# Optimization experiments

Measured on AMD Instinct MI355X. Metric: run time of the kernel, lower is better.

## Reference

```python
import jax, jax.numpy as jnp
import numpy as np

NH, NL, NPNT = 8, 4, 4          # heads, levels, points
NQ, BS, NK, D, DFFN = 100, 8, 18, 256, 1024
SPATIAL = np.array([[92, 92], [46, 46], [23, 23], [12, 12]], np.int32)
LEN_MEM = int((SPATIAL[:, 0] * SPATIAL[:, 1]).sum())  # 11253


def _layernorm(x, g, b):
    m = x.mean(-1, keepdims=True)
    v = ((x - m) ** 2).mean(-1, keepdims=True)
    return (x - m) / jnp.sqrt(v + 1e-5) * g + b


def _mha(xq, xk, xv, in_w, in_b, out_w, out_b):
    # torch nn.MultiheadAttention semantics, inputs (S, B, D)
    S, B, d = xq.shape
    dh = d // NH
    wq, wk, wv = jnp.split(in_w, 3, axis=0)
    bq, bk, bv = jnp.split(in_b, 3, axis=0)
    def proj(x, w, b):
        return (x @ w.T + b).reshape(x.shape[0], B, NH, dh).transpose(1, 2, 0, 3)
    q = proj(xq, wq, bq) * (1.0 / np.sqrt(dh))
    k = proj(xk, wk, bk)
    v = proj(xv, wv, bv)
    att = jax.nn.softmax(jnp.einsum('bhqd,bhkd->bhqk', q, k), axis=-1)
    o = jnp.einsum('bhqk,bhkd->bhqd', att, v).transpose(2, 0, 1, 3).reshape(S, B, d)
    return o @ out_w.T + out_b


def _bilinear(v_l, loc):
    # v_l: (bs,H,W,NH,dh); loc: (bs,Lq,NH,P,2) normalized [0,1]
    # matches F.grid_sample(align_corners=False, padding_mode='zeros')
    bs, H, W, nh, dh = v_l.shape
    x = loc[..., 0] * W - 0.5
    y = loc[..., 1] * H - 0.5
    x0 = jnp.floor(x); y0 = jnp.floor(y)
    lx = x - x0; ly = y - y0
    b_idx = jnp.arange(bs)[:, None, None, None]
    h_idx = jnp.arange(nh)[None, None, :, None]
    def corner(xa, ya, w):
        valid = (xa >= 0) & (xa < W) & (ya >= 0) & (ya < H)
        xi = jnp.clip(xa, 0, W - 1).astype(jnp.int32)
        yi = jnp.clip(ya, 0, H - 1).astype(jnp.int32)
        return v_l[b_idx, yi, xi, h_idx] * (w * valid)[..., None]
    return (corner(x0, y0, (1 - lx) * (1 - ly)) + corner(x0 + 1, y0, lx * (1 - ly))
            + corner(x0, y0 + 1, (1 - lx) * ly) + corner(x0 + 1, y0 + 1, lx * ly))


def _msda(q, rp, mem, pad_mask, ss, off_w, off_b, aw_w, aw_b, val_w, val_b, outp_w, outp_b):
    bs, Lq, d = q.shape
    dh = d // NH
    value = mem @ val_w.T + val_b
    value = jnp.where(pad_mask[..., None], 0.0, value).reshape(bs, -1, NH, dh)
    off = (q @ off_w.T + off_b).reshape(bs, Lq, NH, NL, NPNT, 2)
    aw = jax.nn.softmax((q @ aw_w.T + aw_b).reshape(bs, Lq, NH, NL * NPNT), -1)
    aw = aw.reshape(bs, Lq, NH, NL, NPNT)
    wh = jnp.asarray(ss[:, ::-1].copy(), jnp.float32)  # offset normalizer (W, H)
    loc = rp[:, :, None, :, None, :] + off / wh[None, None, None, :, None, :]
    out = jnp.zeros((bs, Lq, NH, dh), q.dtype)
    start = 0
    for l in range(NL):
        H, W = int(ss[l, 0]), int(ss[l, 1])
        v_l = value[:, start:start + H * W].reshape(bs, H, W, NH, dh)
        start += H * W
        samp = _bilinear(v_l, loc[:, :, :, l])          # (bs,Lq,NH,P,dh)
        out = out + (samp * aw[:, :, :, l, :, None]).sum(3)
    return out.reshape(bs, Lq, d) @ outp_w.T + outp_b


def _forward(tgt_pose, pos, ref_points, memory, w_in_w, w_in_b, w_out_w, w_out_b,
             a_in_w, a_in_b, a_out_w, a_out_b, off_w, off_b, aw_w, aw_b,
             val_w, val_b, outp_w, outp_b, wn_g, wn_b, an_g, an_b,
             n1_g, n1_b, n2_g, n2_b, l1_w, l1_b, l2_w, l2_b,
             spatial_shapes, level_start_index, padding_mask):
    ss = np.asarray(jax.device_get(spatial_shapes))
    nq, bs, nk, d = tgt_pose.shape
    # within-group self-attn over the nk keypoint tokens.
    # NOTE: with_pos_embed mutates tgt_pose in place in the torch code, so
    # q = k = v = tgt + pos and the residual also uses tgt + pos (faithful).
    t = tgt_pose + pos
    x = t.reshape(nq * bs, nk, d).transpose(1, 0, 2)   # (nk, nq*bs, d)
    a1 = _mha(x, x, x, w_in_w, w_in_b, w_out_w, w_out_b)
    t = _layernorm(t + a1.transpose(1, 0, 2).reshape(nq, bs, nk, d), wn_g, wn_b)
    # across-group self-attn over the nq groups
    x2 = t.reshape(nq, bs * nk, d)
    a2 = _mha(x2, x2, x2, a_in_w, a_in_b, a_out_w, a_out_b)
    t = _layernorm(t + a2.reshape(nq, bs, nk, d), an_g, an_b)
    # MSDeformAttn cross-attention (in-place pos add again, faithful)
    t = t + pos
    q = t.transpose(1, 0, 2, 3).reshape(bs, nq * nk, d)
    rp = jnp.swapaxes(ref_points, 0, 1)                # (bs, nq*nk, NL, 2)
    mem = jnp.swapaxes(memory, 0, 1)                   # (bs, LEN_MEM, d)
    c = _msda(q, rp, mem, padding_mask, ss, off_w, off_b, aw_w, aw_b,
              val_w, val_b, outp_w, outp_b)
    c = c.reshape(bs, nq, nk, d).transpose(1, 0, 2, 3)
    t = _layernorm(t + c, n1_g, n1_b)
    # FFN (dropout is identity in eval)
    h = jax.nn.relu(t @ l1_w.T + l1_b)
    return _layernorm(t + (h @ l2_w.T + l2_b), n2_g, n2_b)


def setup_inputs() -> dict:
    key = jax.random.key(0)
    ks = jax.random.split(key, 16)
    p = lambda k, shape: jax.random.normal(k, shape, jnp.float32) * 0.02
    lsi = np.concatenate([[0], np.cumsum(SPATIAL[:, 0] * SPATIAL[:, 1])[:-1]]).astype(np.int32)
    return {
        'tgt_pose': jax.random.normal(ks[0], (NQ, BS, NK, D), jnp.float32),
        'pos': jax.random.normal(ks[1], (NQ, BS, NK, D), jnp.float32),
        'ref_points': jax.random.uniform(ks[2], (NQ * NK, BS, NL, 2), jnp.float32),
        'memory': jax.random.normal(ks[3], (LEN_MEM, BS, D), jnp.float32),
        'w_in_w': p(ks[4], (3 * D, D)), 'w_in_b': jnp.zeros((3 * D,)),
        'w_out_w': p(ks[5], (D, D)), 'w_out_b': jnp.zeros((D,)),
        'a_in_w': p(ks[6], (3 * D, D)), 'a_in_b': jnp.zeros((3 * D,)),
        'a_out_w': p(ks[7], (D, D)), 'a_out_b': jnp.zeros((D,)),
        'off_w': p(ks[8], (NH * NL * NPNT * 2, D)),
        'off_b': jax.random.uniform(ks[9], (NH * NL * NPNT * 2,), jnp.float32, -2.0, 2.0),
        'aw_w': p(ks[10], (NH * NL * NPNT, D)), 'aw_b': jnp.zeros((NH * NL * NPNT,)),
        'val_w': p(ks[11], (D, D)), 'val_b': jnp.zeros((D,)),
        'outp_w': p(ks[12], (D, D)), 'outp_b': jnp.zeros((D,)),
        'wn_g': jnp.ones((D,)), 'wn_b': jnp.zeros((D,)),
        'an_g': jnp.ones((D,)), 'an_b': jnp.zeros((D,)),
        'n1_g': jnp.ones((D,)), 'n1_b': jnp.zeros((D,)),
        'n2_g': jnp.ones((D,)), 'n2_b': jnp.zeros((D,)),
        'l1_w': p(ks[13], (DFFN, D)), 'l1_b': jnp.zeros((DFFN,)),
        'l2_w': p(ks[14], (D, DFFN)), 'l2_b': jnp.zeros((D,)),
        'spatial_shapes': jnp.asarray(SPATIAL),
        'level_start_index': jnp.asarray(lsi),
        'padding_mask': jnp.zeros((BS, LEN_MEM), bool),
    }


def reference(tgt_pose, pos, ref_points, memory, w_in_w, w_in_b, w_out_w, w_out_b,
              a_in_w, a_in_b, a_out_w, a_out_b, off_w, off_b, aw_w, aw_b,
              val_w, val_b, outp_w, outp_b, wn_g, wn_b, an_g, an_b,
              n1_g, n1_b, n2_g, n2_b, l1_w, l1_b, l2_w, l2_b,
              spatial_shapes, level_start_index, padding_mask):
    return _forward(tgt_pose, pos, ref_points, memory, w_in_w, w_in_b, w_out_w, w_out_b,
                    a_in_w, a_in_b, a_out_w, a_out_b, off_w, off_b, aw_w, aw_b,
                    val_w, val_b, outp_w, outp_b, wn_g, wn_b, an_g, an_b,
                    n1_g, n1_b, n2_g, n2_b, l1_w, l1_b, l2_w, l2_b,
                    spatial_shapes, level_start_index, padding_mask)
```

## Files before the change

kernel.cpp:

```cpp
#include <hip/hip_runtime.h>
#include <math.h>

#define NH_ 8
#define D_ 256
#define NK_ 18
#define NQ_ 100
#define BS_ 8
#define LQ_ 1800
#define LEN_MEM_ 11253
#define NTOK_ 14400

typedef short bf16x8 __attribute__((ext_vector_type(8)));
typedef float f32x4 __attribute__((ext_vector_type(4)));
typedef unsigned short ushort;

__device__ inline ushort f2bf(float f) {
    unsigned int u = __builtin_bit_cast(unsigned int, f);
    unsigned int r = (u + 0x7fffu + ((u >> 16) & 1u)) >> 16;
    return (ushort)r;
}
__device__ inline float bf2f_hi(unsigned int u) {
    unsigned int i = u & 0xffff0000u;
    return __builtin_bit_cast(float, i);
}
__device__ inline float bf2f_lo(unsigned int u) {
    unsigned int i = u << 16;
    return __builtin_bit_cast(float, i);
}
__device__ inline int packbf2(float a, float b) {
    return (int)f2bf(a) | ((int)f2bf(b) << 16);
}

__global__ __launch_bounds__(256)
void wcvt_kernel(const float* s0, const float* s1, const float* s2, const float* s3,
                 const float* s4, const float* s5, const float* s6, const float* s7,
                 const float* s8, const float* s9, ushort* dst) {
    const int sizes[10] = {196608,65536,196608,65536,65536,32768,65536,65536,262144,262144};
    const int offs[10]  = {0,196608,262144,458752,524288,589824,622592,688128,753664,1015808};
    int ti = blockIdx.y;
    const float* s;
    switch (ti) {
        case 0: s = s0; break; case 1: s = s1; break; case 2: s = s2; break;
        case 3: s = s3; break; case 4: s = s4; break; case 5: s = s5; break;
        case 6: s = s6; break; case 7: s = s7; break; case 8: s = s8; break;
        default: s = s9; break;
    }
    int n = sizes[ti];
    int i = (blockIdx.x * 256 + threadIdx.x) * 8;
    if (i >= n) return;
    ushort* d = dst + offs[ti] + i;
    float4 f0 = *(const float4*)(s + i);
    float4 f1 = *(const float4*)(s + i + 4);
    int4 val;
    val.x = packbf2(f0.x, f0.y);
    val.y = packbf2(f0.z, f0.w);
    val.z = packbf2(f1.x, f1.y);
    val.w = packbf2(f1.z, f1.w);
    *(int4*)d = val;
}

__global__ __launch_bounds__(256)
void addcvt_kernel(const float* __restrict__ a, const float* __restrict__ b,
                   float* __restrict__ c, ushort* __restrict__ cbf, int n4) {
    int i = blockIdx.x * blockDim.x + threadIdx.x;
    if (i >= n4) return;
    float4 av = ((const float4*)a)[i];
    float4 bv = ((const float4*)b)[i];
    float4 cv;
    cv.x = av.x + bv.x; cv.y = av.y + bv.y; cv.z = av.z + bv.z; cv.w = av.w + bv.w;
    ((float4*)c)[i] = cv;
    uint2 p;
    p.x = (unsigned int)packbf2(cv.x, cv.y);
    p.y = (unsigned int)packbf2(cv.z, cv.w);
    *(uint2*)(cbf + (size_t)i * 4) = p;
}

template<int MODE, bool RELU, bool A_F32, bool OUT_BF16, int BN, int WAVES, int R>
__global__ __launch_bounds__(WAVES * 64)
void gemmw_kernel(const void* __restrict__ Av, const ushort* __restrict__ W,
                  const float* __restrict__ bias, void* __restrict__ Cv,
                  int M, int N, const unsigned char* __restrict__ mask) {
    constexpr int K = 256;
    constexpr int NT = BN / 16;
    __shared__ ushort Ws[32 * BN * 8];
    const int tid = threadIdx.x;
    const int m0 = blockIdx.x * (WAVES * 16 * R);
    const int n0 = blockIdx.y * BN;

    for (int c = tid; c < 32 * BN; c += WAVES * 64) {
        int kc = c & 31, n = c >> 5;
        int dst = kc * BN + (n ^ (kc & 7));
        *(int4*)(Ws + dst * 8) = *(const int4*)(W + (long)(n0 + n) * K + kc * 8);
    }
    __syncthreads();

    const int wv = tid >> 6, lane = tid & 63, fr = lane & 15, hi = lane >> 4;
    const int wm0 = m0 + wv * (16 * R);
    long arow[R];
#pragma unroll
    for (int r = 0; r < R; ++r) {
        int gr = wm0 + r * 16 + fr;
        if (gr > M - 1) gr = M - 1;
        if (MODE == 2) {
            int b = gr / LQ_; int lq = gr - b * LQ_;
            int q = lq / NK_; int kk = lq - q * NK_;
            arow[r] = (long)q * (BS_ * NK_) + b * NK_ + kk;
        } else {
            arow[r] = gr;
        }
    }

    f32x4 acc[R][NT];
#pragma unroll
    for (int r = 0; r < R; ++r)
#pragma unroll
        for (int t = 0; t < NT; ++t) acc[r][t] = f32x4{0.f, 0.f, 0.f, 0.f};

    if (A_F32) {
        const float* ap[R];
        float4 p0[R], p1[R];
#pragma unroll
        for (int r = 0; r < R; ++r) {
            ap[r] = (const float*)Av + arow[r] * (long)K + hi * 8;
            p0[r] = *(const float4*)ap[r];
            p1[r] = *(const float4*)(ap[r] + 4);
        }
#pragma unroll
        for (int ks = 0; ks < 8; ++ks) {
            bf16x8 cur[R];
#pragma unroll
            for (int r = 0; r < R; ++r) {
                int4 v;
                v.x = packbf2(p0[r].x, p0[r].y); v.y = packbf2(p0[r].z, p0[r].w);
                v.z = packbf2(p1[r].x, p1[r].y); v.w = packbf2(p1[r].z, p1[r].w);
                cur[r] = __builtin_bit_cast(bf16x8, v);
                if (ks < 7) {
                    p0[r] = *(const float4*)(ap[r] + (ks + 1) * 32);
                    p1[r] = *(const float4*)(ap[r] + (ks + 1) * 32 + 4);
                }
            }
            const int kc = ks * 4 + hi;
            const ushort* wb = Ws + ((kc * BN) + (fr ^ (kc & 7))) * 8;
#pragma unroll
            for (int t = 0; t < NT; ++t) {
                bf16x8 wf = *(const bf16x8*)(wb + t * 128);
#pragma unroll
                for (int r = 0; r < R; ++r)
                    acc[r][t] = __builtin_amdgcn_mfma_f32_16x16x32_bf16(cur[r], wf, acc[r][t], 0, 0, 0);
            }
        }
    } else {
        const ushort* ap[R];
        bf16x8 afrag[R];
#pragma unroll
        for (int r = 0; r < R; ++r) {
            ap[r] = (const ushort*)Av + arow[r] * (long)K + hi * 8;
            afrag[r] = *(const bf16x8*)ap[r];
        }
#pragma unroll
        for (int ks = 0; ks < 8; ++ks) {
            bf16x8 cur[R];
#pragma unroll
            for (int r = 0; r < R; ++r) {
                cur[r] = afrag[r];
                if (ks < 7) afrag[r] = *(const bf16x8*)(ap[r] + (ks + 1) * 32);
            }
            const int kc = ks * 4 + hi;
            const ushort* wb = Ws + ((kc * BN) + (fr ^ (kc & 7))) * 8;
#pragma unroll
            for (int t = 0; t < NT; ++t) {
                bf16x8 wf = *(const bf16x8*)(wb + t * 128);
#pragma unroll
                for (int r = 0; r < R; ++r)
                    acc[r][t] = __builtin_amdgcn_mfma_f32_16x16x32_bf16(cur[r], wf, acc[r][t], 0, 0, 0);
            }
        }
    }

#pragma unroll
    for (int r = 0; r < R; ++r) {
#pragma unroll
        for (int rr = 0; rr < 4; ++rr) {
            int gm = wm0 + r * 16 + hi * 4 + rr;
            if (gm >= M) continue;
            long orow = gm;
            bool zero = false;
            if (MODE == 1) {
                if (mask && mask[(size_t)(gm & 7) * LEN_MEM_ + (gm >> 3)]) zero = true;
            } else if (MODE == 3) {
                int b = gm / LQ_; int lq = gm - b * LQ_;
                int q = lq / NK_; int kk = lq - q * NK_;
                orow = (long)q * (BS_ * NK_) + b * NK_ + kk;
            }
#pragma unroll
            for (int t = 0; t < NT; ++t) {
                int gn = n0 + t * 16 + fr;
                float v = acc[r][t][rr] + bias[gn];
                if (RELU) v = fmaxf(v, 0.f);
                if (zero) v = 0.f;
                if (OUT_BF16) ((ushort*)Cv)[orow * (long)N + gn] = f2bf(v);
                else ((float*)Cv)[orow * (long)N + gn] = v;
            }
        }
    }
}

template<int MODE, bool RELU, bool A_F32, bool OUT_BF16>
__global__ __launch_bounds__(256)
void gemm_kernel(const void* __restrict__ Av, const ushort* __restrict__ W,
                 const float* __restrict__ bias, void* __restrict__ Cv,
                 int M, int N, int K, const unsigned char* __restrict__ mask) {
    constexpr int AST = 72;
    __shared__ ushort As[128 * AST];
    __shared__ ushort Bs[128 * AST];
    const int m0 = blockIdx.x * 128, n0 = blockIdx.y * 128;
    const int tid = threadIdx.x;
    const int w = tid >> 6, lane = tid & 63;
    const int wr = w >> 1, wc = w & 1;
    const int fr = lane & 15, hi = lane >> 4;
    f32x4 acc[4][4];
#pragma unroll
    for (int i = 0; i < 4; ++i)
#pragma unroll
        for (int j = 0; j < 4; ++j) acc[i][j] = f32x4{0.f, 0.f, 0.f, 0.f};

    const int srow = tid >> 1, shalf = tid & 1;
    long arow = 0;
    const bool avalid = (m0 + srow) < M;
    {
        int gr = m0 + srow;
        if (gr >= M) gr = M - 1;
        arow = gr;
    }

    for (int k0 = 0; k0 < K; k0 += 64) {
        ushort* ad = As + srow * AST + shalf * 32;
        if (avalid) {
            const ushort* ap = (const ushort*)Av + arow * (long)K + k0 + shalf * 32;
#pragma unroll
            for (int i = 0; i < 4; ++i) *(int4*)(ad + i * 8) = *(const int4*)(ap + i * 8);
        } else {
            int4 z = make_int4(0, 0, 0, 0);
#pragma unroll
            for (int i = 0; i < 4; ++i) *(int4*)(ad + i * 8) = z;
        }
        {
            const ushort* wp = W + (long)(n0 + srow) * K + k0 + shalf * 32;
            ushort* bd = Bs + srow * AST + shalf * 32;
#pragma unroll
            for (int i = 0; i < 4; ++i) *(int4*)(bd + i * 8) = *(const int4*)(wp + i * 8);
        }
        __syncthreads();
#pragma unroll
        for (int kb = 0; kb < 2; ++kb) {
            bf16x8 af[4], bfr[4];
#pragma unroll
            for (int i = 0; i < 4; ++i)
                af[i] = *(const bf16x8*)(As + (wr * 64 + i * 16 + fr) * AST + kb * 32 + hi * 8);
#pragma unroll
            for (int j = 0; j < 4; ++j)
                bfr[j] = *(const bf16x8*)(Bs + (wc * 64 + j * 16 + fr) * AST + kb * 32 + hi * 8);
#pragma unroll
            for (int i = 0; i < 4; ++i)
#pragma unroll
                for (int j = 0; j < 4; ++j)
                    acc[i][j] = __builtin_amdgcn_mfma_f32_16x16x32_bf16(af[i], bfr[j], acc[i][j], 0, 0, 0);
        }
        __syncthreads();
    }

#pragma unroll
    for (int i = 0; i < 4; ++i) {
#pragma unroll
        for (int r = 0; r < 4; ++r) {
            int gm = m0 + wr * 64 + i * 16 + hi * 4 + r;
            if (gm >= M) continue;
#pragma unroll
            for (int j = 0; j < 4; ++j) {
                int gn = n0 + wc * 64 + j * 16 + fr;
                float v = acc[i][j][r] + bias[gn];
                if (RELU) v = fmaxf(v, 0.f);
                if (OUT_BF16) ((ushort*)Cv)[(long)gm * N + gn] = f2bf(v);
                else ((float*)Cv)[(long)gm * N + gn] = v;
            }
        }
    }
}

template<int S, int SP, int HPB>
__global__ __launch_bounds__(256)
void mattn_kernel(const ushort* __restrict__ qkv, ushort* __restrict__ outb,
                  int rsG, int rsS) {
    constexpr int SPk = ((SP + 31) / 32) * 32;
    constexpr int KST = 40;
    constexpr int PST = SPk + 8;
    constexpr int NT = SP / 16;
    constexpr int NB = HPB * NT;
    constexpr int HB = 8 / HPB;
    __shared__ ushort KsA[HPB * SP * KST];
    __shared__ ushort VtA[HPB * 32 * PST];
    __shared__ ushort PA [HPB * SP * PST];

    const int tid = threadIdx.x;
    const int g = blockIdx.x / HB;
    const int hbase = (blockIdx.x % HB) * HPB;

    for (int idx = tid; idx < HPB * S * 4; idx += 256) {
        int hh = idx / (S * 4); int rem = idx - hh * (S * 4);
        int j = rem >> 2, q = rem & 3;
        const ushort* base = qkv + ((size_t)g * rsG + (size_t)j * rsS) * 768 + (hbase + hh) * 32 + q * 8;
        uint4 kv = *(const uint4*)(base + 256);
        ushort* kd = KsA + hh * (SP * KST) + j * KST + q * 8;
        *(uint2*)kd = make_uint2(kv.x, kv.y);
        *(uint2*)(kd + 4) = make_uint2(kv.z, kv.w);
        uint4 vv = *(const uint4*)(base + 512);
        ushort* vt = VtA + hh * (32 * PST) + j;
        unsigned int uu[4] = {vv.x, vv.y, vv.z, vv.w};
#pragma unroll
        for (int e = 0; e < 4; ++e) {
            vt[(q * 8 + e * 2    ) * PST] = (ushort)(uu[e] & 0xffff);
            vt[(q * 8 + e * 2 + 1) * PST] = (ushort)(uu[e] >> 16);
        }
    }
    for (int idx = tid; idx < HPB * 32 * (SPk - S); idx += 256) {
        int hh = idx / (32 * (SPk - S)); int rem = idx - hh * (32 * (SPk - S));
        int d = rem / (SPk - S); int c = S + rem - d * (SPk - S);
        VtA[hh * 32 * PST + d * PST + c] = 0;
    }
    if constexpr (SPk > SP) {
        constexpr int PW = SPk - SP;
        for (int idx = tid; idx < HPB * SP * PW; idx += 256) {
            int hh = idx / (SP * PW); int rem = idx - hh * (SP * PW);
            int rrow = rem / PW; int c = SP + rem - rrow * PW;
            PA[hh * SP * PST + rrow * PST + c] = 0;
        }
    }
    __syncthreads();

    const int wv = tid >> 6, lane = tid & 63, fr = lane & 15, hi = lane >> 4;
    for (int band = wv; band < NB; band += 4) {
        const int hh = band / NT, mb = band - (band / NT) * NT;
        const int h = hbase + hh;
        const ushort* Ks = KsA + hh * (SP * KST);
        const ushort* Vt = VtA + hh * (32 * PST);
        ushort* P = PA + hh * (SP * PST);

        int sq = mb * 16 + fr; if (sq > S - 1) sq = S - 1;
        bf16x8 qf = *(const bf16x8*)(qkv + ((size_t)g * rsG + (size_t)sq * rsS) * 768 + h * 32 + hi * 8);
        f32x4 sc[NT];
#pragma unroll
        for (int t = 0; t < NT; ++t) {
            bf16x8 kf = *(const bf16x8*)(Ks + (t * 16 + fr) * KST + hi * 8);
            sc[t] = __builtin_amdgcn_mfma_f32_16x16x32_bf16(qf, kf, f32x4{0.f, 0.f, 0.f, 0.f}, 0, 0, 0);
        }
#pragma unroll
        for (int t = 0; t < NT; ++t) {
            bool valid = (t * 16 + fr) < S;
#pragma unroll
            for (int r = 0; r < 4; ++r)
                sc[t][r] = valid ? sc[t][r] * 0.17677669529663687f : -1e30f;
        }
#pragma unroll
        for (int r = 0; r < 4; ++r) {
            float m = sc[0][r];
#pragma unroll
            for (int t = 1; t < NT; ++t) m = fmaxf(m, sc[t][r]);
            m = fmaxf(m, __shfl_xor(m, 1)); m = fmaxf(m, __shfl_xor(m, 2));
            m = fmaxf(m, __shfl_xor(m, 4)); m = fmaxf(m, __shfl_xor(m, 8));
            float e[NT]; float sum = 0.f;
#pragma unroll
            for (int t = 0; t < NT; ++t) { e[t] = __expf(sc[t][r] - m); sum += e[t]; }
            sum += __shfl_xor(sum, 1); sum += __shfl_xor(sum, 2);
            sum += __shfl_xor(sum, 4); sum += __shfl_xor(sum, 8);
            float inv = 1.f / sum;
            int row = mb * 16 + hi * 4 + r;
#pragma unroll
            for (int t = 0; t < NT; ++t)
                P[row * PST + t * 16 + fr] = f2bf(e[t] * inv);
        }
        f32x4 o0 = {0.f, 0.f, 0.f, 0.f}, o1 = {0.f, 0.f, 0.f, 0.f};
#pragma unroll
        for (int kb = 0; kb < SPk / 32; ++kb) {
            bf16x8 pf = *(const bf16x8*)(P + (mb * 16 + fr) * PST + kb * 32 + hi * 8);
            bf16x8 v0 = *(const bf16x8*)(Vt + fr * PST + kb * 32 + hi * 8);
            bf16x8 v1 = *(const bf16x8*)(Vt + (16 + fr) * PST + kb * 32 + hi * 8);
            o0 = __builtin_amdgcn_mfma_f32_16x16x32_bf16(pf, v0, o0, 0, 0, 0);
            o1 = __builtin_amdgcn_mfma_f32_16x16x32_bf16(pf, v1, o1, 0, 0, 0);
        }
#pragma unroll
        for (int r = 0; r < 4; ++r) {
            int s = mb * 16 + hi * 4 + r;
            if (s < S) {
                size_t ob = ((size_t)g * rsG + (size_t)s * rsS) * 256 + h * 32;
                outb[ob + fr] = f2bf(o0[r]);
                outb[ob + 16 + fr] = f2bf(o1[r]);
            }
        }
    }
}

__global__ __launch_bounds__(256)
void addln_kernel(const float* __restrict__ base, const float* __restrict__ delta,
                  const float* __restrict__ gamma, const float* __restrict__ beta,
                  const float* __restrict__ pos,
                  float* __restrict__ out, ushort* __restrict__ obf, int M) {
    int row = blockIdx.x * 4 + (threadIdx.x >> 6);
    int lane = threadIdx.x & 63;
    if (row >= M) return;
    const float* pb = base + (size_t)row * 256;
    const float* pd = delta + (size_t)row * 256;
    float v[4]; float s = 0.f;
#pragma unroll
    for (int i = 0; i < 4; ++i) { int c = lane + i * 64; v[i] = pb[c] + pd[c]; s += v[i]; }
#pragma unroll
    for (int off = 32; off; off >>= 1) s += __shfl_xor(s, off);
    float mean = s * (1.f / 256.f);
    float var = 0.f;
#pragma unroll
    for (int i = 0; i < 4; ++i) { float d = v[i] - mean; var += d * d; }
#pragma unroll
    for (int off = 32; off; off >>= 1) var += __shfl_xor(var, off);
    var *= (1.f / 256.f);
    float rstd = rsqrtf(var + 1e-5f);
#pragma unroll
    for (int i = 0; i < 4; ++i) {
        int c = lane + i * 64;
        float o = (v[i] - mean) * rstd * gamma[c] + beta[c];
        if (pos) o += pos[(size_t)row * 256 + c];
        out[(size_t)row * 256 + c] = o;
        if (obf) obf[(size_t)row * 256 + c] = f2bf(o);
    }
}

__global__ __launch_bounds__(256)
void msda_kernel(const float* __restrict__ offb, const float* __restrict__ aw,
                 const ushort* __restrict__ val, const float* __restrict__ refp,
                 const int* __restrict__ spatial, const int* __restrict__ lsi,
                 ushort* __restrict__ samp) {
    const int unit = blockIdx.x * 32 + (threadIdx.x >> 3);
    const int lane8 = threadIdx.x & 7;
    const int base8 = (threadIdx.x & 63) & 56;
    const int h = unit & 7;
    const int t = unit >> 3;
    const int lq = t % LQ_;
    const int b = t / LQ_;
    const size_t row = (size_t)b * LQ_ + lq;

    float2 lg = *(const float2*)(aw + row * 128 + h * 16 + lane8 * 2);
    float m = fmaxf(lg.x, lg.y);
    m = fmaxf(m, __shfl_xor(m, 1)); m = fmaxf(m, __shfl_xor(m, 2)); m = fmaxf(m, __shfl_xor(m, 4));
    float e0 = __expf(lg.x - m), e1 = __expf(lg.y - m);
    float s = e0 + e1;
    s += __shfl_xor(s, 1); s += __shfl_xor(s, 2); s += __shfl_xor(s, 4);
    float inv = 1.f / s;
    float w0 = e0 * inv, w1 = e1 * inv;

    float4 of = *(const float4*)(offb + row * 256 + h * 32 + lane8 * 4);

    const float* rp = refp + ((size_t)lq * BS_ + b) * 8;
    float4 rp0 = *(const float4*)rp;
    float4 rp1 = *(const float4*)(rp + 4);

    float acc[4] = {0.f, 0.f, 0.f, 0.f};

#pragma unroll 1
    for (int lvl = 0; lvl < 4; ++lvl) {
        int H = spatial[lvl * 2], W = spatial[lvl * 2 + 1];
        int st = lsi[lvl];
        float rpx = (lvl == 0) ? rp0.x : (lvl == 1) ? rp0.z : (lvl == 2) ? rp1.x : rp1.z;
        float rpy = (lvl == 0) ? rp0.y : (lvl == 1) ? rp0.w : (lvl == 2) ? rp1.y : rp1.w;
        const ushort* vb = val + ((size_t)st * 8 + b) * 256 + h * 32 + lane8 * 4;
        float fW = (float)W, fH = (float)H;
#pragma unroll
        for (int p = 0; p < 4; ++p) {
            float ox_ = (p & 1) ? of.z : of.x;
            float oy_ = (p & 1) ? of.w : of.y;
            float wp_ = (p & 1) ? w1 : w0;
            int src = base8 + lvl * 2 + (p >> 1);
            float ox  = __shfl(ox_, src);
            float oy  = __shfl(oy_, src);
            float wpt = __shfl(wp_, src);

            float x = rpx * fW + ox - 0.5f;
            float y = rpy * fH + oy - 0.5f;
            float x0f = floorf(x), y0f = floorf(y);
            float lx = x - x0f, ly = y - y0f;
            int x0 = (int)x0f, y0 = (int)y0f;
            int xc0 = min(max(x0, 0), W - 1), xc1 = min(max(x0 + 1, 0), W - 1);
            int yc0 = min(max(y0, 0), H - 1), yc1 = min(max(y0 + 1, 0), H - 1);
            float vx0 = (x0 >= 0 && x0 < W) ? 1.f : 0.f;
            float vx1 = (x0 >= -1 && x0 + 1 < W) ? 1.f : 0.f;
            float vy0 = (y0 >= 0 && y0 < H) ? 1.f : 0.f;
            float vy1 = (y0 >= -1 && y0 + 1 < H) ? 1.f : 0.f;
            float w00 = wpt * (1.f - lx) * (1.f - ly) * vx0 * vy0;
            float w10 = wpt * lx * (1.f - ly) * vx1 * vy0;
            float w01 = wpt * (1.f - lx) * ly * vx0 * vy1;
            float w11 = wpt * lx * ly * vx1 * vy1;
            uint2 u00 = *(const uint2*)(vb + (size_t)(yc0 * W + xc0) * 2048);
            uint2 u10 = *(const uint2*)(vb + (size_t)(yc0 * W + xc1) * 2048);
            uint2 u01 = *(const uint2*)(vb + (size_t)(yc1 * W + xc0) * 2048);
            uint2 u11 = *(const uint2*)(vb + (size_t)(yc1 * W + xc1) * 2048);
            acc[0] += w00 * bf2f_lo(u00.x) + w10 * bf2f_lo(u10.x)
                    + w01 * bf2f_lo(u01.x) + w11 * bf2f_lo(u11.x);
            acc[1] += w00 * bf2f_hi(u00.x) + w10 * bf2f_hi(u10.x)
                    + w01 * bf2f_hi(u01.x) + w11 * bf2f_hi(u11.x);
            acc[2] += w00 * bf2f_lo(u00.y) + w10 * bf2f_lo(u10.y)
                    + w01 * bf2f_lo(u01.y) + w11 * bf2f_lo(u11.y);
            acc[3] += w00 * bf2f_hi(u00.y) + w10 * bf2f_hi(u10.y)
                    + w01 * bf2f_hi(u01.y) + w11 * bf2f_hi(u11.y);
        }
    }
    size_t o = row * 256 + h * 32 + lane8 * 4;
    uint2 pk;
    pk.x = (unsigned int)packbf2(acc[0], acc[1]);
    pk.y = (unsigned int)packbf2(acc[2], acc[3]);
    *(uint2*)(samp + o) = pk;
}

extern "C" void kernel_launch(void* const* d_in, const int* in_sizes, int n_in,
                              void* d_out, int out_size, void* d_ws, size_t ws_size,
                              hipStream_t stream) {
    const float* tgt     = (const float*)d_in[0];
    const float* pos     = (const float*)d_in[1];
    const float* refp    = (const float*)d_in[2];
    const float* memory  = (const float*)d_in[3];
    const float* w_in_w  = (const float*)d_in[4];
    const float* w_in_b  = (const float*)d_in[5];
    const float* w_out_w = (const float*)d_in[6];
    const float* w_out_b = (const float*)d_in[7];
    const float* a_in_w  = (const float*)d_in[8];
    const float* a_in_b  = (const float*)d_in[9];
    const float* a_out_w = (const float*)d_in[10];
    const float* a_out_b = (const float*)d_in[11];
    const float* off_w   = (const float*)d_in[12];
    const float* off_b   = (const float*)d_in[13];
    const float* aw_w    = (const float*)d_in[14];
    const float* aw_b    = (const float*)d_in[15];
    const float* val_w   = (const float*)d_in[16];
    const float* val_b   = (const float*)d_in[17];
    const float* outp_w  = (const float*)d_in[18];
    const float* outp_b  = (const float*)d_in[19];
    const float* wn_g    = (const float*)d_in[20];
    const float* wn_b    = (const float*)d_in[21];
    const float* an_g    = (const float*)d_in[22];
    const float* an_b    = (const float*)d_in[23];
    const float* n1_g    = (const float*)d_in[24];
    const float* n1_b    = (const float*)d_in[25];
    const float* n2_g    = (const float*)d_in[26];
    const float* n2_b    = (const float*)d_in[27];
    const float* l1_w    = (const float*)d_in[28];
    const float* l1_b    = (const float*)d_in[29];
    const float* l2_w    = (const float*)d_in[30];
    const float* l2_b    = (const float*)d_in[31];
    const int*   spatial = (const int*)d_in[32];
    const int*   lsi     = (const int*)d_in[33];
    const unsigned char* pmask = (const unsigned char*)d_in[34];
    float* out = (float*)d_out;

    float*  T      = (float*)d_ws;
    ushort* Tbf    = (ushort*)(T + 3686400);
    ushort* B16    = Tbf + 3686400;
    ushort* CBbf   = B16 + 11059200;
    ushort* VALbf  = CBbf + 3686400;
    ushort* SAMPbf = VALbf + 23046144;
    ushort* Hbf    = SAMPbf + 3686400;
    ushort* WB     = Hbf + 14745600;
    float*  OFF    = (float*)(WB + 1277952);
    float*  AW     = OFF + 3686400;

    ushort* WB_win  = WB + 0;
    ushort* WB_wout = WB + 196608;
    ushort* WB_ain  = WB + 262144;
    ushort* WB_aout = WB + 458752;
    ushort* WB_off  = WB + 524288;
    ushort* WB_aw   = WB + 589824;
    ushort* WB_val  = WB + 622592;
    ushort* WB_outp = WB + 688128;
    ushort* WB_l1   = WB + 753664;
    ushort* WB_l2   = WB + 1015808;

    const int n4 = NTOK_ * 256 / 4;

    wcvt_kernel<<<dim3(128, 10), 256, 0, stream>>>(
        w_in_w, w_out_w, a_in_w, a_out_w, off_w, aw_w, val_w, outp_w, l1_w, l2_w, WB);
    addcvt_kernel<<<n4 / 256, 256, 0, stream>>>(tgt, pos, T, Tbf, n4);
    gemmw_kernel<0, false, false, true, 64, 4, 2><<<dim3(113, 12), 256, 0, stream>>>(
        Tbf, WB_win, w_in_b, B16, NTOK_, 768, nullptr);
    mattn_kernel<18, 32, 4><<<800 * 2, 256, 0, stream>>>(B16, CBbf, 18, 1);
    gemmw_kernel<0, false, false, false, 64, 4, 2><<<dim3(113, 4), 256, 0, stream>>>(
        CBbf, WB_wout, w_out_b, OFF, NTOK_, 256, nullptr);
    addln_kernel<<<NTOK_ / 4, 256, 0, stream>>>(T, OFF, wn_g, wn_b, nullptr, T, Tbf, NTOK_);
    gemmw_kernel<0, false, false, true, 64, 4, 2><<<dim3(113, 12), 256, 0, stream>>>(
        Tbf, WB_ain, a_in_b, B16, NTOK_, 768, nullptr);
    mattn_kernel<100, 112, 1><<<144 * 8, 256, 0, stream>>>(B16, CBbf, 1, 144);
    gemmw_kernel<0, false, false, false, 64, 4, 2><<<dim3(113, 4), 256, 0, stream>>>(
        CBbf, WB_aout, a_out_b, OFF, NTOK_, 256, nullptr);
    addln_kernel<<<NTOK_ / 4, 256, 0, stream>>>(T, OFF, an_g, an_b, pos, T, Tbf, NTOK_);
    gemmw_kernel<1, false, true, true, 128, 8, 2><<<dim3(352, 2), 512, 0, stream>>>(
        memory, WB_val, val_b, VALbf, 90024, 256, pmask);
    gemmw_kernel<2, false, false, false, 64, 4, 2><<<dim3(113, 4), 256, 0, stream>>>(
        Tbf, WB_off, off_b, OFF, NTOK_, 256, nullptr);
    gemmw_kernel<2, false, false, false, 64, 4, 2><<<dim3(113, 2), 256, 0, stream>>>(
        Tbf, WB_aw, aw_b, AW, NTOK_, 128, nullptr);
    msda_kernel<<<3600, 256, 0, stream>>>(OFF, AW, VALbf, refp, spatial, lsi, SAMPbf);
    gemmw_kernel<3, false, false, false, 64, 4, 2><<<dim3(113, 4), 256, 0, stream>>>(
        SAMPbf, WB_outp, outp_b, OFF, NTOK_, 256, nullptr);
    addln_kernel<<<NTOK_ / 4, 256, 0, stream>>>(T, OFF, n1_g, n1_b, nullptr, T, Tbf, NTOK_);
    gemmw_kernel<0, true, false, true, 64, 4, 2><<<dim3(113, 16), 256, 0, stream>>>(
        Tbf, WB_l1, l1_b, Hbf, NTOK_, 1024, nullptr);
    gemm_kernel<0, false, false, false><<<dim3(113, 2), 256, 0, stream>>>(
        Hbf, WB_l2, l2_b, OFF, NTOK_, 256, 1024, nullptr);
    addln_kernel<<<NTOK_ / 4, 256, 0, stream>>>(T, OFF, n2_g, n2_b, nullptr, out, nullptr, NTOK_);
}
```

Before: 345.9 us.

## Co-schedule value and QKV GEMMs, fuse offset/weight GEMMs, use bf16 residual deltas

Merges the large value-projection GEMM with the first self-attention in-projection GEMM into a single launch that interleaves blocks of both. Also merges the sampling-offset and attention-weight projections into one launch. The projection outputs feeding the add+LayerNorm kernels are now written in bf16, and the LayerNorm kernel is vectorised with float4 loads and stores. This cuts launch count and the traffic of the intermediate tensors, at the cost of bf16 rounding on the residual deltas and a different tile shape for the QKV GEMM.

```diff
diff --git a/kernel.cpp b/kernel.cpp
--- a/kernel.cpp
+++ b/kernel.cpp
@@ -76,16 +76,15 @@
 }
 
 template<int MODE, bool RELU, bool A_F32, bool OUT_BF16, int BN, int WAVES, int R>
-__global__ __launch_bounds__(WAVES * 64)
-void gemmw_kernel(const void* __restrict__ Av, const ushort* __restrict__ W,
-                  const float* __restrict__ bias, void* __restrict__ Cv,
-                  int M, int N, const unsigned char* __restrict__ mask) {
+__device__ __forceinline__
+void gemmw_body(int bx, int by, const void* __restrict__ Av, const ushort* __restrict__ W,
+                const float* __restrict__ bias, void* __restrict__ Cv,
+                int M, int N, const unsigned char* __restrict__ mask, ushort* Ws) {
     constexpr int K = 256;
     constexpr int NT = BN / 16;
-    __shared__ ushort Ws[32 * BN * 8];
     const int tid = threadIdx.x;
-    const int m0 = blockIdx.x * (WAVES * 16 * R);
-    const int n0 = blockIdx.y * BN;
+    const int m0 = bx * (WAVES * 16 * R);
+    const int n0 = by * BN;
 
     for (int c = tid; c < 32 * BN; c += WAVES * 64) {
         int kc = c & 31, n = c >> 5;
@@ -203,6 +202,49 @@
             }
         }
     }
+}
+
+template<int MODE, bool RELU, bool A_F32, bool OUT_BF16, int BN, int WAVES, int R>
+__global__ __launch_bounds__(WAVES * 64)
+void gemmw_kernel(const void* __restrict__ Av, const ushort* __restrict__ W,
+                  const float* __restrict__ bias, void* __restrict__ Cv,
+                  int M, int N, const unsigned char* __restrict__ mask) {
+    __shared__ ushort Ws[32 * BN * 8];
+    gemmw_body<MODE, RELU, A_F32, OUT_BF16, BN, WAVES, R>(
+        blockIdx.x, blockIdx.y, Av, W, bias, Cv, M, N, mask, Ws);
+}
+
+__global__ __launch_bounds__(512)
+void fusedqv_kernel(const float* __restrict__ memA, const ushort* __restrict__ Wv,
+                    const float* __restrict__ bv, ushort* __restrict__ Cval,
+                    const unsigned char* __restrict__ mask,
+                    const ushort* __restrict__ Aq, const ushort* __restrict__ Wq,
+                    const float* __restrict__ bq, ushort* __restrict__ Cq) {
+    __shared__ ushort Ws[32 * 128 * 8];
+    int idx = blockIdx.x;
+    int g3 = idx / 3, r3 = idx - g3 * 3;
+    if (r3 < 2) {
+        int v = g3 * 2 + r3;
+        gemmw_body<1, false, true, true, 128, 8, 2>(v >> 1, v & 1, memA, Wv, bv, Cval,
+                                                    90024, 256, mask, Ws);
+    } else {
+        int q = g3;
+        if (q < 342)
+            gemmw_body<0, false, false, true, 128, 8, 2>(q % 57, q / 57, Aq, Wq, bq, Cq,
+                                                         NTOK_, 768, nullptr, Ws);
+    }
+}
+
+__global__ __launch_bounds__(256)
+void fusedoa_kernel(const ushort* __restrict__ A,
+                    const ushort* __restrict__ Woff, const float* __restrict__ boff, float* __restrict__ Coff,
+                    const ushort* __restrict__ Waw, const float* __restrict__ baw, float* __restrict__ Caw) {
+    __shared__ ushort Ws[32 * 64 * 8];
+    int by = blockIdx.y;
+    if (by < 4)
+        gemmw_body<2, false, false, false, 64, 4, 2>(blockIdx.x, by, A, Woff, boff, Coff, NTOK_, 256, nullptr, Ws);
+    else
+        gemmw_body<2, false, false, false, 64, 4, 2>(blockIdx.x, by - 4, A, Waw, baw, Caw, NTOK_, 128, nullptr, Ws);
 }
 
 template<int MODE, bool RELU, bool A_F32, bool OUT_BF16>
@@ -400,18 +442,22 @@
 }
 
 __global__ __launch_bounds__(256)
-void addln_kernel(const float* __restrict__ base, const float* __restrict__ delta,
+void addln_kernel(const float* __restrict__ base, const ushort* __restrict__ delta,
                   const float* __restrict__ gamma, const float* __restrict__ beta,
                   const float* __restrict__ pos,
                   float* __restrict__ out, ushort* __restrict__ obf, int M) {
     int row = blockIdx.x * 4 + (threadIdx.x >> 6);
     int lane = threadIdx.x & 63;
     if (row >= M) return;
-    const float* pb = base + (size_t)row * 256;
-    const float* pd = delta + (size_t)row * 256;
-    float v[4]; float s = 0.f;
-#pragma unroll
-    for (int i = 0; i < 4; ++i) { int c = lane + i * 64; v[i] = pb[c] + pd[c]; s += v[i]; }
+    const size_t rb = (size_t)row * 256 + lane * 4;
+    float4 bv = *(const float4*)(base + rb);
+    uint2 du = *(const uint2*)(delta + rb);
+    float v[4];
+    v[0] = bv.x + bf2f_lo(du.x);
+    v[1] = bv.y + bf2f_hi(du.x);
+    v[2] = bv.z + bf2f_lo(du.y);
+    v[3] = bv.w + bf2f_hi(du.y);
+    float s = v[0] + v[1] + v[2] + v[3];
 #pragma unroll
     for (int off = 32; off; off >>= 1) s += __shfl_xor(s, off);
     float mean = s * (1.f / 256.f);
@@ -422,13 +468,24 @@
     for (int off = 32; off; off >>= 1) var += __shfl_xor(var, off);
     var *= (1.f / 256.f);
     float rstd = rsqrtf(var + 1e-5f);
-#pragma unroll
-    for (int i = 0; i < 4; ++i) {
-        int c = lane + i * 64;
-        float o = (v[i] - mean) * rstd * gamma[c] + beta[c];
-        if (pos) o += pos[(size_t)row * 256 + c];
-        out[(size_t)row * 256 + c] = o;
-        if (obf) obf[(size_t)row * 256 + c] = f2bf(o);
+    float4 gv = *(const float4*)(gamma + lane * 4);
+    float4 bev = *(const float4*)(beta + lane * 4);
+    float o[4];
+    o[0] = (v[0] - mean) * rstd * gv.x + bev.x;
+    o[1] = (v[1] - mean) * rstd * gv.y + bev.y;
+    o[2] = (v[2] - mean) * rstd * gv.z + bev.z;
+    o[3] = (v[3] - mean) * rstd * gv.w + bev.w;
+    if (pos) {
+        float4 pv = *(const float4*)(pos + rb);
+        o[0] += pv.x; o[1] += pv.y; o[2] += pv.z; o[3] += pv.w;
+    }
+    float4 ov; ov.x = o[0]; ov.y = o[1]; ov.z = o[2]; ov.w = o[3];
+    *(float4*)(out + rb) = ov;
+    if (obf) {
+        uint2 p;
+        p.x = (unsigned int)packbf2(o[0], o[1]);
+        p.y = (unsigned int)packbf2(o[2], o[3]);
+        *(uint2*)(obf + rb) = p;
     }
 }
 
@@ -567,6 +624,7 @@
     ushort* WB     = Hbf + 14745600;
     float*  OFF    = (float*)(WB + 1277952);
     float*  AW     = OFF + 3686400;
+    ushort* OFFbf  = (ushort*)(AW + 1843200);
 
     ushort* WB_win  = WB + 0;
     ushort* WB_wout = WB + 196608;
@@ -584,31 +642,27 @@
     wcvt_kernel<<<dim3(128, 10), 256, 0, stream>>>(
         w_in_w, w_out_w, a_in_w, a_out_w, off_w, aw_w, val_w, outp_w, l1_w, l2_w, WB);
     addcvt_kernel<<<n4 / 256, 256, 0, stream>>>(tgt, pos, T, Tbf, n4);
-    gemmw_kernel<0, false, false, true, 64, 4, 2><<<dim3(113, 12), 256, 0, stream>>>(
-        Tbf, WB_win, w_in_b, B16, NTOK_, 768, nullptr);
+    fusedqv_kernel<<<3 * 352, 512, 0, stream>>>(
+        memory, WB_val, val_b, VALbf, pmask, Tbf, WB_win, w_in_b, B16);
     mattn_kernel<18, 32, 4><<<800 * 2, 256, 0, stream>>>(B16, CBbf, 18, 1);
-    gemmw_kernel<0, false, false, false, 64, 4, 2><<<dim3(113, 4), 256, 0, stream>>>(
-        CBbf, WB_wout, w_out_b, OFF, NTOK_, 256, nullptr);
-    addln_kernel<<<NTOK_ / 4, 256, 0, stream>>>(T, OFF, wn_g, wn_b, nullptr, T, Tbf, NTOK_);
+    gemmw_kernel<0, false, false, true, 64, 4, 2><<<dim3(113, 4), 256, 0, stream>>>(
+        CBbf, WB_wout, w_out_b, OFFbf, NTOK_, 256, nullptr);
+    addln_kernel<<<NTOK_ / 4, 256, 0, stream>>>(T, OFFbf, wn_g, wn_b, nullptr, T, Tbf, NTOK_);
     gemmw_kernel<0, false, false, true, 64, 4, 2><<<dim3(113, 12), 256, 0, stream>>>(
         Tbf, WB_ain, a_in_b, B16, NTOK_, 768, nullptr);
     mattn_kernel<100, 112, 1><<<144 * 8, 256, 0, stream>>>(B16, CBbf, 1, 144);
-    gemmw_kernel<0, false, false, false, 64, 4, 2><<<dim3(113, 4), 256, 0, stream>>>(
-        CBbf, WB_aout, a_out_b, OFF, NTOK_, 256, nullptr);
-    addln_kernel<<<NTOK_ / 4, 256, 0, stream>>>(T, OFF, an_g, an_b, pos, T, Tbf, NTOK_);
-    gemmw_kernel<1, false, true, true, 128, 8, 2><<<dim3(352, 2), 512, 0, stream>>>(
-        memory, WB_val, val_b, VALbf, 90024, 256, pmask);
-    gemmw_kernel<2, false, false, false, 64, 4, 2><<<dim3(113, 4), 256, 0, stream>>>(
-        Tbf, WB_off, off_b, OFF, NTOK_, 256, nullptr);
-    gemmw_kernel<2, false, false, false, 64, 4, 2><<<dim3(113, 2), 256, 0, stream>>>(
-        Tbf, WB_aw, aw_b, AW, NTOK_, 128, nullptr);
+    gemmw_kernel<0, false, false, true, 64, 4, 2><<<dim3(113, 4), 256, 0, stream>>>(
+        CBbf, WB_aout, a_out_b, OFFbf, NTOK_, 256, nullptr);
+    addln_kernel<<<NTOK_ / 4, 256, 0, stream>>>(T, OFFbf, an_g, an_b, pos, T, Tbf, NTOK_);
+    fusedoa_kernel<<<dim3(113, 6), 256, 0, stream>>>(
+        Tbf, WB_off, off_b, OFF, WB_aw, aw_b, AW);
     msda_kernel<<<3600, 256, 0, stream>>>(OFF, AW, VALbf, refp, spatial, lsi, SAMPbf);
-    gemmw_kernel<3, false, false, false, 64, 4, 2><<<dim3(113, 4), 256, 0, stream>>>(
-        SAMPbf, WB_outp, outp_b, OFF, NTOK_, 256, nullptr);
-    addln_kernel<<<NTOK_ / 4, 256, 0, stream>>>(T, OFF, n1_g, n1_b, nullptr, T, Tbf, NTOK_);
+    gemmw_kernel<3, false, false, true, 64, 4, 2><<<dim3(113, 4), 256, 0, stream>>>(
+        SAMPbf, WB_outp, outp_b, OFFbf, NTOK_, 256, nullptr);
+    addln_kernel<<<NTOK_ / 4, 256, 0, stream>>>(T, OFFbf, n1_g, n1_b, nullptr, T, Tbf, NTOK_);
     gemmw_kernel<0, true, false, true, 64, 4, 2><<<dim3(113, 16), 256, 0, stream>>>(
         Tbf, WB_l1, l1_b, Hbf, NTOK_, 1024, nullptr);
-    gemm_kernel<0, false, false, false><<<dim3(113, 2), 256, 0, stream>>>(
-        Hbf, WB_l2, l2_b, OFF, NTOK_, 256, 1024, nullptr);
-    addln_kernel<<<NTOK_ / 4, 256, 0, stream>>>(T, OFF, n2_g, n2_b, nullptr, out, nullptr, NTOK_);
-}
+    gemm_kernel<0, false, false, true><<<dim3(113, 2), 256, 0, stream>>>(
+        Hbf, WB_l2, l2_b, OFFbf, NTOK_, 256, 1024, nullptr);
+    addln_kernel<<<NTOK_ / 4, 256, 0, stream>>>(T, OFFbf, n2_g, n2_b, nullptr, out, nullptr, NTOK_);
+}
```

Result: faster. 321.2 us (-7.1%).
